# Kernel optimization log

Measured on AMD Instinct MI355X. Metric: run time of the kernel, lower is better.

Reference implementation:

```python
import jax, jax.numpy as jnp
import numpy as np

# dims
B, T = 256, 64
N_AG, N_FEAT = 10, 4
X_DIM, X_PERM, X_STATIC = 44, 40, 10
HID, XEMB, NHID = 128, 32, 8
E = N_AG * (N_AG - 1)           # 90 directed edges (off-diagonal)
GEMB = NHID * E                 # 720 graph embedding per sample/step
RNN_IN = XEMB + 1 + GEMB        # 753
A_IN = X_STATIC + GEMB          # 730 (x_emb_size2==0 in GraphNN branch)
O_IN = XEMB + X_STATIC + 1 + GEMB  # 763

_off = np.ones((N_AG, N_AG)) - np.eye(N_AG)
RECV = jnp.asarray(np.where(_off)[0])  # rel_rec one-hot == gather by receiver idx
SEND = jnp.asarray(np.where(_off)[1])  # rel_send one-hot == gather by sender idx


def setup_inputs() -> dict:
    key = jax.random.key(0)
    ks = jax.random.split(key, 32)
    w = lambda k, shape: jax.random.normal(k, shape, jnp.float32) * 0.05
    return {
        'x': jax.random.normal(ks[0], (B, T + 1, X_DIM), jnp.float32),
        'x_demo': jax.random.normal(ks[1], (B, X_STATIC), jnp.float32),
        'f_treatment': jax.random.uniform(ks[2], (B, T + 1, 1), jnp.float32),
        'h0': jax.random.normal(ks[3], (B, HID), jnp.float32),
        # x2emb (Linear 4->32), x_static2emb (Linear 10->10)
        'W_x2emb': w(ks[4], (XEMB, X_DIM - X_PERM)), 'b_x2emb': w(ks[5], (XEMB,)),
        'W_stat': w(ks[6], (X_STATIC, X_STATIC)), 'b_stat': w(ks[7], (X_STATIC,)),
        # NRI-style MLP1 (node): 4->8->8 ; MLP2 (edge): 16->8->8
        'W_m1a': w(ks[8], (NHID, N_FEAT)), 'b_m1a': w(ks[9], (NHID,)),
        'W_m1b': w(ks[10], (NHID, NHID)), 'b_m1b': w(ks[11], (NHID,)),
        'W_m2a': w(ks[12], (NHID, 2 * NHID)), 'b_m2a': w(ks[13], (NHID,)),
        'W_m2b': w(ks[14], (NHID, NHID)), 'b_m2b': w(ks[15], (NHID,)),
        # treatment head: Linear(730->128)+ReLU, then Linear(128->1, no bias)
        'W_a1': w(ks[16], (HID, A_IN)), 'b_a1': w(ks[17], (HID,)),
        'W_a2': w(ks[18], (1, HID)),
        # outcome head: Linear(763->128)+ReLU, then Linear(128->1, no bias)
        'W_o1': w(ks[19], (HID, O_IN)), 'b_o1': w(ks[20], (HID,)),
        'W_o2': w(ks[21], (1, HID)),
        # GRUCell(753 -> 128)
        'W_ih': w(ks[22], (3 * HID, RNN_IN)), 'b_ih': w(ks[23], (3 * HID,)),
        'W_hh': w(ks[24], (3 * HID, HID)), 'b_hh': w(ks[25], (3 * HID,)),
    }


def reference(x, x_demo, f_treatment, h0, W_x2emb, b_x2emb, W_stat, b_stat,
              W_m1a, b_m1a, W_m1b, b_m1b, W_m2a, b_m2a, W_m2b, b_m2b,
              W_a1, b_a1, W_a2, W_o1, b_o1, W_o2, W_ih, b_ih, W_hh, b_hh):
    xt = x[:, :T]                       # (B,T,44); len_time = x.size(1)-1
    treat = f_treatment[:, :T]          # (B,T,1)
    demo = x_demo @ W_stat.T + b_stat   # (B,10) static embedding
    demoT = jnp.broadcast_to(demo[:, None], (B, T, X_STATIC))

    # --- GNN(x_permuted): mlp1 per node, node2edge gather, mlp2 per edge ---
    xa = xt[..., :X_PERM].reshape(B, T, N_AG, N_FEAT)
    h1 = jax.nn.elu(xa @ W_m1a.T + b_m1a)
    h1 = jax.nn.elu(h1 @ W_m1b.T + b_m1b)         # (B,T,N_AG,8); BN in eval = identity
    edges = jnp.concatenate([h1[:, :, RECV], h1[:, :, SEND]], axis=-1)  # (B,T,E,16)
    h2 = jax.nn.elu(edges @ W_m2a.T + b_m2a)
    h2 = jax.nn.elu(h2 @ W_m2b.T + b_m2b)         # (B,T,E,8)
    gemb = h2.reshape(B, T, GEMB)                 # (B,T,720)

    xemb = xt[..., X_PERM:] @ W_x2emb.T + b_x2emb  # (B,T,32)

    # --- treatment (a_or_ipw) head; dropout identity in eval ---
    a_in = jnp.concatenate([demoT, gemb], axis=-1)          # (B,T,730)
    a_out = jax.nn.relu(a_in @ W_a1.T + b_a1) @ W_a2.T      # (B,T,1)

    # --- outcome head ---
    o_in = jnp.concatenate([xemb, demoT, treat, gemb], axis=-1)  # (B,T,763)
    y_out = jax.nn.relu(o_in @ W_o1.T + b_o1) @ W_o2.T           # (B,T,1)

    # --- GRUCell recurrence over time ---
    rnn_in = jnp.concatenate([xemb, treat, gemb], axis=-1)  # (B,T,753)
    gi = rnn_in @ W_ih.T + b_ih                             # precompute input proj (B,T,3H)

    def step(h, g):
        gh = h @ W_hh.T + b_hh
        i_r, i_z, i_n = jnp.split(g, 3, axis=-1)
        h_r, h_z, h_n = jnp.split(gh, 3, axis=-1)
        r = jax.nn.sigmoid(i_r + h_r)
        z = jax.nn.sigmoid(i_z + h_z)
        n = jnp.tanh(i_n + r * h_n)
        h_new = (1.0 - z) * n + z * h
        return h_new, h_new

    _, hs = jax.lax.scan(step, h0, jnp.swapaxes(gi, 0, 1))
    hs = jnp.swapaxes(hs, 0, 1)                             # (B,T,128)

    return jnp.concatenate([a_out, y_out, hs], axis=-1)     # (B,T,130)
```

## Files before the change

### kernel.cpp

```cpp
#include <hip/hip_runtime.h>
#include <hip/hip_bf16.h>
#include <math.h>

#define BB     256
#define TT     64
#define BT     (BB*TT)
#define XD     44
#define XP     40
#define XS     10
#define HID    128
#define XEMB   32
#define NHID   8
#define NAG    10
#define NEDGE  90
#define GEMB   720
#define KF     768
#define NTOT   640


typedef __bf16  bf16_t;
typedef __bf16  bf16x4 __attribute__((ext_vector_type(4)));
typedef __bf16  bf16x8 __attribute__((ext_vector_type(8)));
typedef float   floatx4 __attribute__((ext_vector_type(4)));
typedef _Float16 half2_t __attribute__((ext_vector_type(2)));
typedef _Float16 half4_t __attribute__((ext_vector_type(4)));
typedef _Float16 half8_t __attribute__((ext_vector_type(8)));

__device__ __forceinline__ float rcp_fast(float x) { return __builtin_amdgcn_rcpf(x); }
__device__ __forceinline__ float sigmoid_fast(float v) { return rcp_fast(1.f + __expf(-v)); }
__device__ __forceinline__ float tanh_fast(float x) { return 1.f - 2.f * rcp_fast(1.f + __expf(2.f * x)); }
__device__ __forceinline__ float elu_fast(float v) { return v > 0.f ? v : __expf(v) - 1.f; }
__device__ __forceinline__ float fdot2f(half2_t a, half2_t b, float acc) {
  return __builtin_amdgcn_fdot2(a, b, acc, false);
}
__device__ __forceinline__ float dot8h(half8_t a, half8_t b, float acc) {
  acc = fdot2f(half2_t{a[0], a[1]}, half2_t{b[0], b[1]}, acc);
  acc = fdot2f(half2_t{a[2], a[3]}, half2_t{b[2], b[3]}, acc);
  acc = fdot2f(half2_t{a[4], a[5]}, half2_t{b[4], b[5]}, acc);
  acc = fdot2f(half2_t{a[6], a[7]}, half2_t{b[6], b[7]}, acc);
  return acc;
}
__device__ __forceinline__ void lds_barrier() {
  asm volatile("s_waitcnt lgkmcnt(0)" ::: "memory");
  __builtin_amdgcn_s_barrier();
}

__global__ __launch_bounds__(256) void prep_kernel(
    const float* __restrict__ Wa1, const float* __restrict__ ba1,
    const float* __restrict__ Wo1, const float* __restrict__ bo1,
    const float* __restrict__ Wih, const float* __restrict__ bih,
    bf16_t* __restrict__ WT, float* __restrict__ bcat) {
  int idx = blockIdx.x * 256 + threadIdx.x;
  if (idx >= NTOT * KF) return;
  int n = idx / KF, k = idx - n * KF;
  float v = 0.f;
  if (n < 128) {
    if (k >= 32 && k < 42)  v = Wa1[n * 730 + (k - 32)];
    else if (k >= 48)       v = Wa1[n * 730 + 10 + (k - 48)];
  } else if (n < 256) {
    int m = n - 128;
    if (k < 43)             v = Wo1[m * 763 + k];
    else if (k >= 48)       v = Wo1[m * 763 + 43 + (k - 48)];
  } else {
    int m = n - 256;
    if (k < 32)             v = Wih[m * 753 + k];
    else if (k == 42)       v = Wih[m * 753 + 32];
    else if (k >= 48)       v = Wih[m * 753 + 33 + (k - 48)];
  }
  WT[n * KF + k] = (bf16_t)v;
  if (k == 0) {
    bcat[n] = (n < 128) ? ba1[n] : (n < 256 ? bo1[n - 128] : bih[n - 256]);
  }
}

__global__ __launch_bounds__(64) void encoder_kernel(
    const float* __restrict__ x, const float* __restrict__ x_demo,
    const float* __restrict__ ftreat,
    const float* __restrict__ Wm1a, const float* __restrict__ bm1a,
    const float* __restrict__ Wm1b, const float* __restrict__ bm1b,
    const float* __restrict__ Wm2a, const float* __restrict__ bm2a,
    const float* __restrict__ Wm2b, const float* __restrict__ bm2b,
    const float* __restrict__ Wx2e, const float* __restrict__ bx2e,
    const float* __restrict__ Wst, const float* __restrict__ bst,
    bf16_t* __restrict__ F) {
  int blk = blockIdx.x;
  int b = blk >> 4, tc = blk & 15;
  int lane = threadIdx.x;

  __shared__ __align__(16) _Float16 h1sp[NAG * 8];
  __shared__ __align__(16) _Float16 w2aR[64];
  __shared__ __align__(16) _Float16 w2aS[64];
  __shared__ __align__(16) _Float16 w2bp[64];
  __shared__ float demoL[XS];

  if (lane < 8) {
    float4 v0 = *(const float4*)(Wm2a + lane * 16);
    float4 v1 = *(const float4*)(Wm2a + lane * 16 + 4);
    float4 v2 = *(const float4*)(Wm2a + lane * 16 + 8);
    float4 v3 = *(const float4*)(Wm2a + lane * 16 + 12);
    *(half8_t*)&w2aR[lane * 8] = half8_t{
        (_Float16)v0.x, (_Float16)v0.y, (_Float16)v0.z, (_Float16)v0.w,
        (_Float16)v1.x, (_Float16)v1.y, (_Float16)v1.z, (_Float16)v1.w};
    *(half8_t*)&w2aS[lane * 8] = half8_t{
        (_Float16)v2.x, (_Float16)v2.y, (_Float16)v2.z, (_Float16)v2.w,
        (_Float16)v3.x, (_Float16)v3.y, (_Float16)v3.z, (_Float16)v3.w};
    float4 u0 = *(const float4*)(Wm2b + lane * 8);
    float4 u1 = *(const float4*)(Wm2b + lane * 8 + 4);
    *(half8_t*)&w2bp[lane * 8] = half8_t{
        (_Float16)u0.x, (_Float16)u0.y, (_Float16)u0.z, (_Float16)u0.w,
        (_Float16)u1.x, (_Float16)u1.y, (_Float16)u1.z, (_Float16)u1.w};
  }
  if (lane < 10) {
    float s = bst[lane];
#pragma unroll
    for (int j = 0; j < 10; j++) s += x_demo[b * XS + j] * Wst[lane * 10 + j];
    demoL[lane] = s;
  }

  half4_t wA[8]; float bA[8];
  half8_t wB1[8]; float bB1[8];
  float bR[8], bG[8];
#pragma unroll
  for (int o = 0; o < 8; o++) {
    float4 v = *(const float4*)(Wm1a + o * 4);
    wA[o] = half4_t{(_Float16)v.x, (_Float16)v.y, (_Float16)v.z, (_Float16)v.w};
    bA[o] = bm1a[o];
    float4 w0 = *(const float4*)(Wm1b + o * 8);
    float4 w1 = *(const float4*)(Wm1b + o * 8 + 4);
    wB1[o] = half8_t{(_Float16)w0.x, (_Float16)w0.y, (_Float16)w0.z, (_Float16)w0.w,
                     (_Float16)w1.x, (_Float16)w1.y, (_Float16)w1.z, (_Float16)w1.w};
    bB1[o] = bm1b[o];
    bR[o] = bm2a[o];
    bG[o] = bm2b[o];
  }
  half4_t wX; float bX;
  {
    float4 v = *(const float4*)(Wx2e + (lane & 31) * 4);
    wX = half4_t{(_Float16)v.x, (_Float16)v.y, (_Float16)v.z, (_Float16)v.w};
    bX = bx2e[lane & 31];
  }
  __syncthreads();
  float demov = (lane >= 32 && lane < 42) ? demoL[lane - 32] : 0.f;

  for (int ti = 0; ti < 4; ti++) {
    int t = tc * 4 + ti;
    int tok = b * TT + t;
    const float* row = x + (size_t)(b * 65 + t) * XD;
    bf16_t* Frow = F + (size_t)tok * KF;

    if (lane < NAG) {
      float4 xa = *(const float4*)(row + lane * 4);
      half2_t x0{(_Float16)xa.x, (_Float16)xa.y};
      half2_t x1{(_Float16)xa.z, (_Float16)xa.w};
      float h1v[8];
#pragma unroll
      for (int o = 0; o < 8; o++) {
        float s = bA[o];
        s = fdot2f(x0, half2_t{wA[o][0], wA[o][1]}, s);
        s = fdot2f(x1, half2_t{wA[o][2], wA[o][3]}, s);
        h1v[o] = elu_fast(s);
      }
      half2_t e0{(_Float16)h1v[0], (_Float16)h1v[1]};
      half2_t e1{(_Float16)h1v[2], (_Float16)h1v[3]};
      half2_t e2{(_Float16)h1v[4], (_Float16)h1v[5]};
      half2_t e3{(_Float16)h1v[6], (_Float16)h1v[7]};
      half8_t hout;
#pragma unroll
      for (int o = 0; o < 8; o++) {
        float s = bB1[o];
        s = fdot2f(e0, half2_t{wB1[o][0], wB1[o][1]}, s);
        s = fdot2f(e1, half2_t{wB1[o][2], wB1[o][3]}, s);
        s = fdot2f(e2, half2_t{wB1[o][4], wB1[o][5]}, s);
        s = fdot2f(e3, half2_t{wB1[o][6], wB1[o][7]}, s);
        hout[o] = (_Float16)elu_fast(s);
      }
      *(half8_t*)&h1sp[lane * 8] = hout;
    }
    __syncthreads();

#pragma unroll
    for (int q = 0; q < 2; q++) {
      int e = lane + 64 * q;
      if (e < NEDGE) {
        int r = (e * 57) >> 9;
        int sd = e - 9 * r;
        sd += (sd >= r) ? 1 : 0;
        half8_t hr = *(const half8_t*)&h1sp[r * 8];
        half8_t hs = *(const half8_t*)&h1sp[sd * 8];
        float av[8];
#pragma unroll
        for (int o = 0; o < 8; o++) {
          half8_t wr8 = *(const half8_t*)&w2aR[o * 8];
          half8_t ws8 = *(const half8_t*)&w2aS[o * 8];
          float s = bR[o];
          s = dot8h(hr, wr8, s);
          s = dot8h(hs, ws8, s);
          av[o] = elu_fast(s);
        }
        half2_t a0{(_Float16)av[0], (_Float16)av[1]};
        half2_t a1{(_Float16)av[2], (_Float16)av[3]};
        half2_t a2{(_Float16)av[4], (_Float16)av[5]};
        half2_t a3{(_Float16)av[6], (_Float16)av[7]};
        union { bf16_t h[8]; uint4 u; } pk;
#pragma unroll
        for (int o = 0; o < 8; o++) {
          half8_t wb8 = *(const half8_t*)&w2bp[o * 8];
          float s = bG[o];
          s = fdot2f(a0, half2_t{wb8[0], wb8[1]}, s);
          s = fdot2f(a1, half2_t{wb8[2], wb8[3]}, s);
          s = fdot2f(a2, half2_t{wb8[4], wb8[5]}, s);
          s = fdot2f(a3, half2_t{wb8[6], wb8[7]}, s);
          pk.h[o] = (bf16_t)elu_fast(s);
        }
        *(uint4*)(Frow + 48 + e * 8) = pk.u;
      }
    }

    float4 xe = *(const float4*)(row + XP);
    if (lane < 32) {
      float s = bX;
      s = fdot2f(half2_t{(_Float16)xe.x, (_Float16)xe.y}, half2_t{wX[0], wX[1]}, s);
      s = fdot2f(half2_t{(_Float16)xe.z, (_Float16)xe.w}, half2_t{wX[2], wX[3]}, s);
      Frow[lane] = (bf16_t)s;
    } else if (lane < 42) {
      Frow[lane] = (bf16_t)demov;
    } else if (lane == 42) {
      Frow[42] = (bf16_t)ftreat[b * 65 + t];
    } else if (lane < 48) {
      Frow[lane] = (bf16_t)0.f;
    }
    __syncthreads();
  }
}

__global__ __launch_bounds__(256) void gemm_kernel(
    const bf16_t* __restrict__ F, const bf16_t* __restrict__ WT,
    const float* __restrict__ bcat, float* __restrict__ Gao,
    float* __restrict__ Gih) {
  __shared__ __align__(16) bf16_t As[128 * 32];
  __shared__ __align__(16) bf16_t Bs[128 * 32];

  int tid  = threadIdx.x;
  int lane = tid & 63;
  int wv   = tid >> 6;
  int wr   = wv >> 1, wc = wv & 1;
  int m0 = blockIdx.x * 128, n0 = blockIdx.y * 128;

  floatx4 acc[4][4];
#pragma unroll
  for (int i = 0; i < 4; i++)
#pragma unroll
    for (int j = 0; j < 4; j++) acc[i][j] = floatx4{0.f, 0.f, 0.f, 0.f};

  int c0 = tid, c1 = tid + 256;
  int r0 = c0 >> 2, p0 = c0 & 3;
  int r1 = c1 >> 2, p1 = c1 & 3;
  int qr = lane >> 4;
  int lr = lane & 15;

  for (int k0 = 0; k0 < KF; k0 += 32) {
    uint4 a0 = *(const uint4*)(F  + (size_t)(m0 + r0) * KF + k0 + p0 * 8);
    uint4 a1 = *(const uint4*)(F  + (size_t)(m0 + r1) * KF + k0 + p1 * 8);
    uint4 b0 = *(const uint4*)(WT + (size_t)(n0 + r0) * KF + k0 + p0 * 8);
    uint4 b1 = *(const uint4*)(WT + (size_t)(n0 + r1) * KF + k0 + p1 * 8);
    __syncthreads();
    ((uint4*)As)[c0] = a0; ((uint4*)As)[c1] = a1;
    ((uint4*)Bs)[c0] = b0; ((uint4*)Bs)[c1] = b1;
    __syncthreads();

    bf16x8 af[4], bf[4];
#pragma unroll
    for (int i = 0; i < 4; i++) {
      af[i] = *(const bf16x8*)(As + (wr * 64 + i * 16 + lr) * 32 + qr * 8);
      bf[i] = *(const bf16x8*)(Bs + (wc * 64 + i * 16 + lr) * 32 + qr * 8);
    }
#pragma unroll
    for (int i = 0; i < 4; i++)
#pragma unroll
      for (int j = 0; j < 4; j++)
        acc[i][j] = __builtin_amdgcn_mfma_f32_16x16x32_bf16(af[i], bf[j], acc[i][j], 0, 0, 0);
  }

#pragma unroll
  for (int i = 0; i < 4; i++) {
#pragma unroll
    for (int j = 0; j < 4; j++) {
      int col = n0 + wc * 64 + j * 16 + lr;
      float bv = bcat[col];
#pragma unroll
      for (int r = 0; r < 4; r++) {
        int row = m0 + wr * 64 + i * 16 + qr * 4 + r;
        float val = acc[i][j][r] + bv;
        if (n0 < 256) {
          Gao[(size_t)row * 256 + col] = val;
        } else {
          int tt = row & 63, bq = row >> 6;
          Gih[(size_t)(tt * 256 + bq) * 384 + (col - 256)] = val;
        }
      }
    }
  }
}

__global__ __launch_bounds__(256) void head_kernel(
    const float* __restrict__ Gao, const float* __restrict__ Wa2,
    const float* __restrict__ Wo2, float* __restrict__ out) {
  int wid  = (blockIdx.x * 256 + threadIdx.x) >> 6;
  int lane = threadIdx.x & 63;
  const float* g = Gao + (size_t)wid * 256;
  float sa = fmaxf(g[lane], 0.f) * Wa2[lane] + fmaxf(g[lane + 64], 0.f) * Wa2[lane + 64];
  float sy = fmaxf(g[128 + lane], 0.f) * Wo2[lane] + fmaxf(g[192 + lane], 0.f) * Wo2[lane + 64];
#pragma unroll
  for (int off = 32; off > 0; off >>= 1) {
    sa += __shfl_down(sa, off, 64);
    sy += __shfl_down(sy, off, 64);
  }
  if (lane == 0) {
    out[(size_t)wid * 130 + 0] = sa;
    out[(size_t)wid * 130 + 1] = sy;
  }
}

__global__ __launch_bounds__(512, 1) void gru_kernel(
    const float* __restrict__ Gih, const float* __restrict__ h0,
    const float* __restrict__ Whh, const float* __restrict__ bhh,
    float* __restrict__ out) {
  int tid  = threadIdx.x;
  int w    = tid >> 6;
  int lane = tid & 63;
  int l15  = lane & 15;
  int quad = lane >> 4;
  int b0   = blockIdx.x * 16;
  int s    = b0 + l15;
  int jb   = w * 16 + quad * 4;

  __shared__ __align__(16) bf16_t hT[2][16 * 136];

  bf16x8 afrag[3][4];
#pragma unroll
  for (int g = 0; g < 3; g++) {
    const float* wrow = Whh + (size_t)(g * 128 + w * 16 + l15) * HID + quad * 8;
#pragma unroll
    for (int ks = 0; ks < 4; ks++) {
      float4 a = *(const float4*)(wrow + ks * 32);
      float4 b = *(const float4*)(wrow + ks * 32 + 4);
      afrag[g][ks] = bf16x8{
          (bf16_t)a.x, (bf16_t)a.y, (bf16_t)a.z, (bf16_t)a.w,
          (bf16_t)b.x, (bf16_t)b.y, (bf16_t)b.z, (bf16_t)b.w};
    }
  }
  floatx4 biasv[3];
#pragma unroll
  for (int g = 0; g < 3; g++) biasv[g] = *(const floatx4*)(bhh + g * 128 + jb);
  floatx4 hprev = *(const floatx4*)(h0 + (size_t)s * HID + jb);

  if (tid < 256) {
    int sq = tid >> 4, u = (tid & 15) * 8;
    const float* hr = h0 + (size_t)(b0 + sq) * HID + u;
    float4 a = *(const float4*)hr;
    float4 b = *(const float4*)(hr + 4);
    *(bf16x8*)&hT[0][sq * 136 + u] = bf16x8{
        (bf16_t)a.x, (bf16_t)a.y, (bf16_t)a.z, (bf16_t)a.w,
        (bf16_t)b.x, (bf16_t)b.y, (bf16_t)b.z, (bf16_t)b.w};
  }

  const float* gbase = Gih + (size_t)s * 384 + jb;
  floatx4 gA[3], gB[3];
#pragma unroll
  for (int g = 0; g < 3; g++) gA[g] = *(const floatx4*)(gbase + g * 128);
#pragma unroll
  for (int g = 0; g < 3; g++) gB[g] = *(const floatx4*)(gbase + 98304 + g * 128);
  __syncthreads();

#define GRU_STEP(T, GREG)                                                      \
  {                                                                            \
    const bf16_t* hb = &hT[(T) & 1][l15 * 136 + quad * 8];                     \
    bf16x8 bfrag[4];                                                           \
    _Pragma("unroll")                                                          \
    for (int ks = 0; ks < 4; ks++) bfrag[ks] = *(const bf16x8*)(hb + ks * 32); \
    floatx4 acc[3];                                                            \
    _Pragma("unroll")                                                          \
    for (int g = 0; g < 3; g++) acc[g] = biasv[g];                             \
    _Pragma("unroll")                                                          \
    for (int ks = 0; ks < 4; ks++)                                             \
      _Pragma("unroll")                                                        \
      for (int g = 0; g < 3; g++)                                              \
        acc[g] = __builtin_amdgcn_mfma_f32_16x16x32_bf16(                      \
            afrag[g][ks], bfrag[ks], acc[g], 0, 0, 0);                         \
    floatx4 hn;                                                                \
    _Pragma("unroll")                                                          \
    for (int r = 0; r < 4; r++) {                                              \
      float rr = sigmoid_fast(GREG[0][r] + acc[0][r]);                         \
      float zz = sigmoid_fast(GREG[1][r] + acc[1][r]);                         \
      float nn = tanh_fast(GREG[2][r] + rr * acc[2][r]);                       \
      hn[r] = (1.f - zz) * nn + zz * hprev[r];                                 \
    }                                                                          \
    hprev = hn;                                                                \
    *(bf16x4*)&hT[((T) + 1) & 1][l15 * 136 + jb] =                             \
        bf16x4{(bf16_t)hn[0], (bf16_t)hn[1], (bf16_t)hn[2], (bf16_t)hn[3]};    \
    float* ob = out + ((size_t)s * TT + (T)) * 130 + 2 + jb;                   \
    *(float2*)ob = float2{hn[0], hn[1]};                                       \
    *(float2*)(ob + 2) = float2{hn[2], hn[3]};                                 \
    if ((T) + 2 < TT) {                                                        \
      const float* gp = gbase + (size_t)((T) + 2) * 98304;                     \
      _Pragma("unroll")                                                        \
      for (int g = 0; g < 3; g++) GREG[g] = *(const floatx4*)(gp + g * 128);   \
    }                                                                          \
    lds_barrier();                                                             \
  }

  for (int t = 0; t < TT; t += 2) {
    GRU_STEP(t, gA);
    GRU_STEP(t + 1, gB);
  }
#undef GRU_STEP
}

extern "C" void kernel_launch(void* const* d_in, const int* in_sizes, int n_in,
                              void* d_out, int out_size, void* d_ws, size_t ws_size,
                              hipStream_t stream) {
  const float* x      = (const float*)d_in[0];
  const float* x_demo = (const float*)d_in[1];
  const float* ftr    = (const float*)d_in[2];
  const float* h0     = (const float*)d_in[3];
  const float* Wx2e   = (const float*)d_in[4];
  const float* bx2e   = (const float*)d_in[5];
  const float* Wst    = (const float*)d_in[6];
  const float* bst    = (const float*)d_in[7];
  const float* Wm1a   = (const float*)d_in[8];
  const float* bm1a   = (const float*)d_in[9];
  const float* Wm1b   = (const float*)d_in[10];
  const float* bm1b   = (const float*)d_in[11];
  const float* Wm2a   = (const float*)d_in[12];
  const float* bm2a   = (const float*)d_in[13];
  const float* Wm2b   = (const float*)d_in[14];
  const float* bm2b   = (const float*)d_in[15];
  const float* Wa1    = (const float*)d_in[16];
  const float* ba1    = (const float*)d_in[17];
  const float* Wa2    = (const float*)d_in[18];
  const float* Wo1    = (const float*)d_in[19];
  const float* bo1    = (const float*)d_in[20];
  const float* Wo2    = (const float*)d_in[21];
  const float* Wih    = (const float*)d_in[22];
  const float* bih    = (const float*)d_in[23];
  const float* Whh    = (const float*)d_in[24];
  const float* bhh    = (const float*)d_in[25];
  float* out = (float*)d_out;

  char* ws = (char*)d_ws;
  bf16_t* F   = (bf16_t*)(ws);
  bf16_t* WT  = (bf16_t*)(ws + 25165824);
  float*  bc  = (float*)(ws + 25165824 + 983040);
  float*  Gao = (float*)(ws + 25165824 + 983040 + 2560);
  float*  Gih = (float*)(ws + 25165824 + 983040 + 2560 + 16777216);

  prep_kernel<<<dim3((NTOT * KF + 255) / 256), dim3(256), 0, stream>>>(
      Wa1, ba1, Wo1, bo1, Wih, bih, WT, bc);
  encoder_kernel<<<dim3(BB * 16), dim3(64), 0, stream>>>(
      x, x_demo, ftr, Wm1a, bm1a, Wm1b, bm1b, Wm2a, bm2a, Wm2b, bm2b,
      Wx2e, bx2e, Wst, bst, F);
  gemm_kernel<<<dim3(BT / 128, NTOT / 128), dim3(256), 0, stream>>>(F, WT, bc, Gao, Gih);
  head_kernel<<<dim3(BT / 4), dim3(256), 0, stream>>>(Gao, Wa2, Wo2, out);
  gru_kernel<<<dim3(BB / 16), dim3(512), 0, stream>>>(Gih, h0, Whh, bhh, out);
}
```

Baseline: 240.6 us.

## Fuse head reduction into GEMM epilogue and load tiles via global_load_lds

Fuses the treatment/outcome head (ReLU, dot with the second-layer weight, row reduction) into the GEMM epilogue using shuffles and a small LDS exchange. This drops the head kernel and the 16 MB intermediate Gao buffer write and read. It also switches the A/B tile loads to direct global-to-LDS loads, so the data no longer passes through registers. The direct loads depend on the per-lane LDS layout produced by global_load_lds matching the old layout.

```diff
diff --git a/kernel.cpp b/kernel.cpp
--- a/kernel.cpp
+++ b/kernel.cpp
@@ -43,6 +43,11 @@
 __device__ __forceinline__ void lds_barrier() {
   asm volatile("s_waitcnt lgkmcnt(0)" ::: "memory");
   __builtin_amdgcn_s_barrier();
+}
+__device__ __forceinline__ void gl16(const bf16_t* g, bf16_t* l) {
+  __builtin_amdgcn_global_load_lds(
+      (const __attribute__((address_space(1))) void*)g,
+      (__attribute__((address_space(3))) void*)l, 16, 0, 0);
 }
 
 __global__ __launch_bounds__(256) void prep_kernel(
@@ -235,10 +240,12 @@
 
 __global__ __launch_bounds__(256) void gemm_kernel(
     const bf16_t* __restrict__ F, const bf16_t* __restrict__ WT,
-    const float* __restrict__ bcat, float* __restrict__ Gao,
-    float* __restrict__ Gih) {
+    const float* __restrict__ bcat, const float* __restrict__ Wa2,
+    const float* __restrict__ Wo2, float* __restrict__ Gih,
+    float* __restrict__ out) {
   __shared__ __align__(16) bf16_t As[128 * 32];
   __shared__ __align__(16) bf16_t Bs[128 * 32];
+  __shared__ float hred[128];
 
   int tid  = threadIdx.x;
   int lane = tid & 63;
@@ -252,20 +259,20 @@
 #pragma unroll
     for (int j = 0; j < 4; j++) acc[i][j] = floatx4{0.f, 0.f, 0.f, 0.f};
 
-  int c0 = tid, c1 = tid + 256;
-  int r0 = c0 >> 2, p0 = c0 & 3;
-  int r1 = c1 >> 2, p1 = c1 & 3;
   int qr = lane >> 4;
   int lr = lane & 15;
 
+  const bf16_t* gA = F  + (size_t)(m0 + wv * 32 + (lane >> 2)) * KF + (lane & 3) * 8;
+  const bf16_t* gB = WT + (size_t)(n0 + wv * 32 + (lane >> 2)) * KF + (lane & 3) * 8;
+  bf16_t* lA = As + (wv * 32) * 32;
+  bf16_t* lB = Bs + (wv * 32) * 32;
+
   for (int k0 = 0; k0 < KF; k0 += 32) {
-    uint4 a0 = *(const uint4*)(F  + (size_t)(m0 + r0) * KF + k0 + p0 * 8);
-    uint4 a1 = *(const uint4*)(F  + (size_t)(m0 + r1) * KF + k0 + p1 * 8);
-    uint4 b0 = *(const uint4*)(WT + (size_t)(n0 + r0) * KF + k0 + p0 * 8);
-    uint4 b1 = *(const uint4*)(WT + (size_t)(n0 + r1) * KF + k0 + p1 * 8);
-    __syncthreads();
-    ((uint4*)As)[c0] = a0; ((uint4*)As)[c1] = a1;
-    ((uint4*)Bs)[c0] = b0; ((uint4*)Bs)[c1] = b1;
+    __syncthreads();
+    gl16(gA + k0,             lA);
+    gl16(gA + 16 * KF + k0,   lA + 16 * 32);
+    gl16(gB + k0,             lB);
+    gl16(gB + 16 * KF + k0,   lB + 16 * 32);
     __syncthreads();
 
     bf16x8 af[4], bf[4];
@@ -281,43 +288,65 @@
         acc[i][j] = __builtin_amdgcn_mfma_f32_16x16x32_bf16(af[i], bf[j], acc[i][j], 0, 0, 0);
   }
 
-#pragma unroll
-  for (int i = 0; i < 4; i++) {
-#pragma unroll
-    for (int j = 0; j < 4; j++) {
-      int col = n0 + wc * 64 + j * 16 + lr;
-      float bv = bcat[col];
-#pragma unroll
-      for (int r = 0; r < 4; r++) {
-        int row = m0 + wr * 64 + i * 16 + qr * 4 + r;
-        float val = acc[i][j][r] + bv;
-        if (n0 < 256) {
-          Gao[(size_t)row * 256 + col] = val;
-        } else {
+  if (n0 >= 256) {
+#pragma unroll
+    for (int i = 0; i < 4; i++) {
+#pragma unroll
+      for (int j = 0; j < 4; j++) {
+        int col = n0 + wc * 64 + j * 16 + lr;
+        float bv = bcat[col];
+#pragma unroll
+        for (int r = 0; r < 4; r++) {
+          int row = m0 + wr * 64 + i * 16 + qr * 4 + r;
           int tt = row & 63, bq = row >> 6;
-          Gih[(size_t)(tt * 256 + bq) * 384 + (col - 256)] = val;
+          Gih[(size_t)(tt * 256 + bq) * 384 + (col - 256)] = acc[i][j][r] + bv;
         }
       }
     }
-  }
-}
-
-__global__ __launch_bounds__(256) void head_kernel(
-    const float* __restrict__ Gao, const float* __restrict__ Wa2,
-    const float* __restrict__ Wo2, float* __restrict__ out) {
-  int wid  = (blockIdx.x * 256 + threadIdx.x) >> 6;
-  int lane = threadIdx.x & 63;
-  const float* g = Gao + (size_t)wid * 256;
-  float sa = fmaxf(g[lane], 0.f) * Wa2[lane] + fmaxf(g[lane + 64], 0.f) * Wa2[lane + 64];
-  float sy = fmaxf(g[128 + lane], 0.f) * Wo2[lane] + fmaxf(g[192 + lane], 0.f) * Wo2[lane + 64];
-#pragma unroll
-  for (int off = 32; off > 0; off >>= 1) {
-    sa += __shfl_down(sa, off, 64);
-    sy += __shfl_down(sy, off, 64);
-  }
-  if (lane == 0) {
-    out[(size_t)wid * 130 + 0] = sa;
-    out[(size_t)wid * 130 + 1] = sy;
+  } else {
+    const float* w2 = (n0 == 0) ? Wa2 : Wo2;
+    int head = (n0 == 0) ? 0 : 1;
+    float v[4][4];
+#pragma unroll
+    for (int i = 0; i < 4; i++)
+#pragma unroll
+      for (int r = 0; r < 4; r++) v[i][r] = 0.f;
+#pragma unroll
+    for (int j = 0; j < 4; j++) {
+      int colh = wc * 64 + j * 16 + lr;
+      float bv = bcat[n0 + colh];
+      float ww = w2[colh];
+#pragma unroll
+      for (int i = 0; i < 4; i++)
+#pragma unroll
+        for (int r = 0; r < 4; r++)
+          v[i][r] += fmaxf(acc[i][j][r] + bv, 0.f) * ww;
+    }
+#pragma unroll
+    for (int off = 8; off > 0; off >>= 1)
+#pragma unroll
+      for (int i = 0; i < 4; i++)
+#pragma unroll
+        for (int r = 0; r < 4; r++)
+          v[i][r] += __shfl_down(v[i][r], off, 64);
+    __syncthreads();
+    if (lr == 0 && wc == 0) {
+#pragma unroll
+      for (int i = 0; i < 4; i++)
+#pragma unroll
+        for (int r = 0; r < 4; r++)
+          hred[wr * 64 + i * 16 + qr * 4 + r] = v[i][r];
+    }
+    __syncthreads();
+    if (lr == 0 && wc == 1) {
+#pragma unroll
+      for (int i = 0; i < 4; i++)
+#pragma unroll
+        for (int r = 0; r < 4; r++) {
+          int row = wr * 64 + i * 16 + qr * 4 + r;
+          out[(size_t)(m0 + row) * 130 + head] = hred[row] + v[i][r];
+        }
+    }
   }
 }
 
@@ -451,15 +480,14 @@
   bf16_t* F   = (bf16_t*)(ws);
   bf16_t* WT  = (bf16_t*)(ws + 25165824);
   float*  bc  = (float*)(ws + 25165824 + 983040);
-  float*  Gao = (float*)(ws + 25165824 + 983040 + 2560);
-  float*  Gih = (float*)(ws + 25165824 + 983040 + 2560 + 16777216);
+  float*  Gih = (float*)(ws + 25165824 + 983040 + 2560);
 
   prep_kernel<<<dim3((NTOT * KF + 255) / 256), dim3(256), 0, stream>>>(
       Wa1, ba1, Wo1, bo1, Wih, bih, WT, bc);
   encoder_kernel<<<dim3(BB * 16), dim3(64), 0, stream>>>(
       x, x_demo, ftr, Wm1a, bm1a, Wm1b, bm1b, Wm2a, bm2a, Wm2b, bm2b,
       Wx2e, bx2e, Wst, bst, F);
-  gemm_kernel<<<dim3(BT / 128, NTOT / 128), dim3(256), 0, stream>>>(F, WT, bc, Gao, Gih);
-  head_kernel<<<dim3(BT / 4), dim3(256), 0, stream>>>(Gao, Wa2, Wo2, out);
+  gemm_kernel<<<dim3(BT / 128, NTOT / 128), dim3(256), 0, stream>>>(
+      F, WT, bc, Wa2, Wo2, Gih, out);
   gru_kernel<<<dim3(BB / 16), dim3(512), 0, stream>>>(Gih, h0, Whh, bhh, out);
 }
```

New measurement: 236.0 us. About the same (-1.9%).
